# Kernel tuning notes

Measured on AMD Instinct MI355X. Metric: run time of the kernel, lower is better.

The kernel has to match this reference:

```python
import jax, jax.numpy as jnp
import numpy as np

N_PAIR = 32
N_ENTI = 36          # VidVRD object classes (+pad)
N_CLS_TOT = 133      # 132 predicate classes + background id 0
NUM_BASE = 92        # split='base' -> pids 1..92
N_CTX = 8
MAX_L = 40           # GeneralAlproCfg.max_txt_len
D = 768


def setup_inputs() -> dict:
    key = jax.random.key(0)
    ks = jax.random.split(key, 11)
    std = 0.02
    return {
        "so_cls_ids": jax.random.randint(ks[0], (N_PAIR, 2), 0, N_ENTI, dtype=jnp.int64),
        "enti_txt_embds": jax.random.normal(ks[1], (N_ENTI, 256), jnp.float32),
        "prefix_embds": jax.random.normal(ks[2], (N_CLS_TOT, 1, D), jnp.float32) * std,
        "suffix_embds": jax.random.normal(ks[3], (N_CLS_TOT, MAX_L - 1 - N_CTX, D), jnp.float32) * std,
        "token_mask": jnp.ones((N_CLS_TOT, MAX_L), jnp.int32),
        "meta_ctx_embds": jax.random.normal(ks[4], (N_CTX, D), jnp.float32) * std,
        "subj_ctx_embds": jax.random.normal(ks[5], (N_CTX, D), jnp.float32) * std,
        "obj_ctx_embds": jax.random.normal(ks[6], (N_CTX, D), jnp.float32) * std,
        "W1": jax.random.normal(ks[7], (512, 256), jnp.float32) * std,
        "b1": jnp.zeros((256,), jnp.float32),
        "W2": jax.random.normal(ks[8], (256, 2 * D), jnp.float32) * std,
    }


def reference(so_cls_ids, enti_txt_embds, prefix_embds, suffix_embds, token_mask,
              meta_ctx_embds, subj_ctx_embds, obj_ctx_embds, W1, b1, W2):
    n_pair = so_cls_ids.shape[0]
    pids = jnp.arange(1, NUM_BASE + 1)                      # split='base'
    n_cls = NUM_BASE

    # entity text-embedding gather + tiny MLP
    s_embd = enti_txt_embds[so_cls_ids[:, 0]]               # [n_pair, 256]
    o_embd = enti_txt_embds[so_cls_ids[:, 1]]
    so = jnp.concatenate([s_embd, o_embd], axis=-1)         # [n_pair, 512]
    h = jax.nn.relu(so @ W1 + b1)                           # [n_pair, 256]
    so_e = h @ W2                                           # [n_pair, 1536]
    s_q, o_q = so_e[:, :D], so_e[:, D:]

    # softmax attention over meta context (keys = values = meta_ctx_embds)
    scale = 1.0 / jnp.sqrt(jnp.asarray(D, jnp.float32))
    s_att = jax.nn.softmax(s_q @ meta_ctx_embds.T * scale, axis=-1) @ meta_ctx_embds  # [n_pair, D]
    o_att = jax.nn.softmax(o_q @ meta_ctx_embds.T * scale, axis=-1) @ meta_ctx_embds

    s_ctx = subj_ctx_embds[None, :, :] + s_att[:, None, :]  # [n_pair, n_ctx, D]
    o_ctx = obj_ctx_embds[None, :, :] + o_att[:, None, :]

    prefix = prefix_embds[pids]                             # [n_cls, 1, D]
    suffix = suffix_embds[pids]                             # [n_cls, L_suf, D]
    l_suf = suffix.shape[1]

    def build(ctx):
        return jnp.concatenate([
            jnp.broadcast_to(prefix[None], (n_pair, n_cls, 1, D)),
            jnp.broadcast_to(ctx[:, None], (n_pair, n_cls, N_CTX, D)),
            jnp.broadcast_to(suffix[None], (n_pair, n_cls, l_suf, D)),
        ], axis=2).reshape(n_pair * n_cls, MAX_L, D)

    subj_token_embds = build(s_ctx)                         # [n_pair*n_cls, MAX_L, D]
    obj_token_embds = build(o_ctx)
    mask = jnp.tile(token_mask[pids], (n_pair, 1))          # [n_pair*n_cls, MAX_L]
    return subj_token_embds, obj_token_embds, mask
```

## Files before the change

kernel.cpp:

```cpp
#include <hip/hip_runtime.h>
#include <hip/hip_bf16.h>

typedef unsigned int u32;
typedef __attribute__((ext_vector_type(4))) float f32x4;

#define NPAIR 32
#define NCLS  92
#define NCTX  8
#define MAXL  40
#define DIM   768
#define LSUF  31

#define MAT_ELEMS 90439680u
#define MASK_BASE 180879360u
#define NBLK_MAT  7360u
#define MASK_F4   29440u
#define NBLK_MASK 154u

__global__ __launch_bounds__(512) void k_mlp_att(
    const int* __restrict__ so_ids,
    const float* __restrict__ enti,
    const float* __restrict__ meta,
    const float* __restrict__ W1,
    const float* __restrict__ b1,
    const float* __restrict__ W2,
    float* __restrict__ att)
{
    const int p = blockIdx.x;
    const int t = threadIdx.x;
    __shared__ float so_vec[512];
    __shared__ float w1part[2][256];
    __shared__ float h[256];
    __shared__ float w2part[2][1536];
    __shared__ float so_e[1536];
    __shared__ float red[8][512];
    __shared__ float probs[8];
    __shared__ int ids[2];

    if (t == 0) {
        bool is64 = true;
        for (int i = 1; i < 64; i += 2) is64 = is64 && (so_ids[i] == 0);
        if (is64) { ids[0] = so_ids[4 * p];     ids[1] = so_ids[4 * p + 2]; }
        else      { ids[0] = so_ids[2 * p];     ids[1] = so_ids[2 * p + 1]; }
    }
    __syncthreads();
    const int s_id = ids[0];
    const int o_id = ids[1];
    so_vec[t] = (t < 256) ? enti[s_id * 256 + t] : enti[o_id * 256 + (t - 256)];
    __syncthreads();

    {
        const int j = t & 255, half = t >> 8;
        const float* w = W1 + (half * 256) * 256 + j;
        const float* sv = so_vec + half * 256;
        float acc = 0.f;
        #pragma unroll 8
        for (int kk = 0; kk < 256; ++kk)
            acc = fmaf(sv[kk], w[(size_t)kk * 256], acc);
        w1part[half][j] = acc;
    }
    __syncthreads();
    if (t < 256) h[t] = fmaxf(w1part[0][t] + w1part[1][t] + b1[t], 0.f);
    __syncthreads();

    {
        const int c = t & 255, khalf = t >> 8;
        float a6[6] = {0.f, 0.f, 0.f, 0.f, 0.f, 0.f};
        const float* w = W2 + (khalf * 128) * 1536 + c;
        const float* hh = h + khalf * 128;
        #pragma unroll 4
        for (int kk = 0; kk < 128; ++kk) {
            const float hk = hh[kk];
            #pragma unroll
            for (int r = 0; r < 6; ++r)
                a6[r] = fmaf(hk, w[(size_t)kk * 1536 + r * 256], a6[r]);
        }
        #pragma unroll
        for (int r = 0; r < 6; ++r) w2part[khalf][r * 256 + c] = a6[r];
    }
    __syncthreads();
    for (int c = t; c < 1536; c += 512) so_e[c] = w2part[0][c] + w2part[1][c];
    __syncthreads();

    const float scale = 0.036084391824351615f;
    for (int which = 0; which < 2; ++which) {
        const float* q = &so_e[which * DIM];
        #pragma unroll
        for (int c = 0; c < 8; ++c) {
            float pp = 0.f;
            for (int d = t; d < DIM; d += 512)
                pp = fmaf(q[d], meta[c * DIM + d], pp);
            red[c][t] = pp;
        }
        __syncthreads();
        for (int s = 256; s > 0; s >>= 1) {
            if (t < s) {
                #pragma unroll
                for (int c = 0; c < 8; ++c)
                    red[c][t] += red[c][t + s];
            }
            __syncthreads();
        }
        if (t == 0) {
            float sc[8], m = -1e30f;
            #pragma unroll
            for (int c = 0; c < 8; ++c) { sc[c] = red[c][0] * scale; m = fmaxf(m, sc[c]); }
            float sum = 0.f;
            #pragma unroll
            for (int c = 0; c < 8; ++c) { sc[c] = expf(sc[c] - m); sum += sc[c]; }
            const float inv = 1.f / sum;
            #pragma unroll
            for (int c = 0; c < 8; ++c) probs[c] = sc[c] * inv;
        }
        __syncthreads();
        for (int d = t; d < DIM; d += 512) {
            float a = 0.f;
            #pragma unroll
            for (int c = 0; c < 8; ++c)
                a = fmaf(probs[c], meta[c * DIM + d], a);
            att[(which * NPAIR + p) * DIM + d] = a;
        }
        __syncthreads();
    }
}

__global__ __launch_bounds__(192) void k_build(
    const float* __restrict__ prefix,
    const float* __restrict__ suffix,
    const int* __restrict__ tok_mask,
    const float* __restrict__ sctx,
    const float* __restrict__ octx,
    const float* __restrict__ att,
    float* __restrict__ out)
{
    const u32 bid = blockIdx.x;
    const u32 t = threadIdx.x;

    if (bid < NBLK_MAT) {
        const u32 which = bid / 3680u;
        const u32 rem = bid - which * 3680u;
        const u32 cls = rem / 40u;
        const u32 tok = rem - cls * 40u;
        const u32 d = t * 4u;

        f32x4 src;
        bool is_ctx = false;
        if (tok == 0u) {
            src = *(const f32x4*)(prefix + (cls + 1u) * DIM + d);
        } else if (tok < 9u) {
            const float* cp = (which ? octx : sctx) + (tok - 1u) * DIM + d;
            src = *(const f32x4*)cp;
            is_ctx = true;
        } else {
            src = *(const f32x4*)(suffix + ((cls + 1u) * LSUF + (tok - 9u)) * DIM + d);
        }

        float* base = out + (size_t)which * MAT_ELEMS + (size_t)(cls * MAXL + tok) * DIM + d;
        const float* ab = att + (size_t)which * NPAIR * DIM + d;
        if (is_ctx) {
            #pragma unroll 4
            for (u32 p = 0; p < NPAIR; ++p) {
                const f32x4 a = *(const f32x4*)(ab + (size_t)p * DIM);
                __builtin_nontemporal_store(src + a,
                    (f32x4*)(base + (size_t)p * (NCLS * MAXL * DIM)));
            }
        } else {
            #pragma unroll 4
            for (u32 p = 0; p < NPAIR; ++p) {
                __builtin_nontemporal_store(src,
                    (f32x4*)(base + (size_t)p * (NCLS * MAXL * DIM)));
            }
        }
    } else {
        const u32 idx4 = (bid - NBLK_MAT) * 192u + t;
        if (idx4 < MASK_F4) {
            const u32 m = idx4 * 4u;
            f32x4 v;
            #pragma unroll
            for (int j = 0; j < 4; ++j) {
                const u32 i = m + (u32)j;
                const u32 rw = i / 40u;
                const u32 tk = i - rw * 40u;
                const u32 cls = rw % 92u;
                v[j] = (float)tok_mask[(cls + 1u) * 40u + tk];
            }
            __builtin_nontemporal_store(v, (f32x4*)(out + MASK_BASE + m));
        }
    }
}

extern "C" void kernel_launch(void* const* d_in, const int* in_sizes, int n_in,
                              void* d_out, int out_size, void* d_ws, size_t ws_size,
                              hipStream_t stream) {
    const int* so_ids     = (const int*)d_in[0];
    const float* enti     = (const float*)d_in[1];
    const float* prefix   = (const float*)d_in[2];
    const float* suffix   = (const float*)d_in[3];
    const int* tok_mask   = (const int*)d_in[4];
    const float* meta     = (const float*)d_in[5];
    const float* sctx     = (const float*)d_in[6];
    const float* octx     = (const float*)d_in[7];
    const float* W1       = (const float*)d_in[8];
    const float* b1       = (const float*)d_in[9];
    const float* W2       = (const float*)d_in[10];
    float* att = (float*)d_ws;

    k_mlp_att<<<dim3(NPAIR), dim3(512), 0, stream>>>(so_ids, enti, meta, W1, b1, W2, att);
    k_build<<<dim3(NBLK_MAT + NBLK_MASK), dim3(192), 0, stream>>>(
        prefix, suffix, tok_mask, sctx, octx, att, (float*)d_out);
}
```

Baseline: 176.1 us.

## Split MLP-attention kernel into three kernels for more block parallelism

Breaks the single 32-block MLP+attention kernel into three launches: the first layer with ReLU, the W2 projection spread over 192 blocks, and the softmax attention over 64 blocks. Intermediates go through workspace buffers. The aim is to spread the serial small-matrix work across more CUs instead of 32 large blocks. The cost is two extra kernel launches and round trips through global memory. The prologue is small next to the large output-writing build kernel, which probably dominates total time.

```diff
diff --git a/kernel.cpp b/kernel.cpp
--- a/kernel.cpp
+++ b/kernel.cpp
@@ -17,24 +17,21 @@
 #define MASK_F4   29440u
 #define NBLK_MASK 154u
 
-__global__ __launch_bounds__(512) void k_mlp_att(
+#define WS_ATT  0u
+#define WS_H    49152u
+#define WS_SOE  57344u
+
+__global__ __launch_bounds__(512) void k_h(
     const int* __restrict__ so_ids,
     const float* __restrict__ enti,
-    const float* __restrict__ meta,
     const float* __restrict__ W1,
     const float* __restrict__ b1,
-    const float* __restrict__ W2,
-    float* __restrict__ att)
+    float* __restrict__ ws)
 {
     const int p = blockIdx.x;
     const int t = threadIdx.x;
     __shared__ float so_vec[512];
     __shared__ float w1part[2][256];
-    __shared__ float h[256];
-    __shared__ float w2part[2][1536];
-    __shared__ float so_e[1536];
-    __shared__ float red[8][512];
-    __shared__ float probs[8];
     __shared__ int ids[2];
 
     if (t == 0) {
@@ -44,83 +41,95 @@
         else      { ids[0] = so_ids[2 * p];     ids[1] = so_ids[2 * p + 1]; }
     }
     __syncthreads();
-    const int s_id = ids[0];
-    const int o_id = ids[1];
-    so_vec[t] = (t < 256) ? enti[s_id * 256 + t] : enti[o_id * 256 + (t - 256)];
-    __syncthreads();
-
-    {
-        const int j = t & 255, half = t >> 8;
-        const float* w = W1 + (half * 256) * 256 + j;
-        const float* sv = so_vec + half * 256;
-        float acc = 0.f;
-        #pragma unroll 8
-        for (int kk = 0; kk < 256; ++kk)
-            acc = fmaf(sv[kk], w[(size_t)kk * 256], acc);
-        w1part[half][j] = acc;
-    }
-    __syncthreads();
-    if (t < 256) h[t] = fmaxf(w1part[0][t] + w1part[1][t] + b1[t], 0.f);
-    __syncthreads();
-
-    {
-        const int c = t & 255, khalf = t >> 8;
-        float a6[6] = {0.f, 0.f, 0.f, 0.f, 0.f, 0.f};
-        const float* w = W2 + (khalf * 128) * 1536 + c;
-        const float* hh = h + khalf * 128;
-        #pragma unroll 4
-        for (int kk = 0; kk < 128; ++kk) {
-            const float hk = hh[kk];
-            #pragma unroll
-            for (int r = 0; r < 6; ++r)
-                a6[r] = fmaf(hk, w[(size_t)kk * 1536 + r * 256], a6[r]);
-        }
-        #pragma unroll
-        for (int r = 0; r < 6; ++r) w2part[khalf][r * 256 + c] = a6[r];
-    }
-    __syncthreads();
-    for (int c = t; c < 1536; c += 512) so_e[c] = w2part[0][c] + w2part[1][c];
-    __syncthreads();
-
-    const float scale = 0.036084391824351615f;
-    for (int which = 0; which < 2; ++which) {
-        const float* q = &so_e[which * DIM];
-        #pragma unroll
-        for (int c = 0; c < 8; ++c) {
-            float pp = 0.f;
-            for (int d = t; d < DIM; d += 512)
-                pp = fmaf(q[d], meta[c * DIM + d], pp);
-            red[c][t] = pp;
-        }
-        __syncthreads();
-        for (int s = 256; s > 0; s >>= 1) {
-            if (t < s) {
-                #pragma unroll
-                for (int c = 0; c < 8; ++c)
-                    red[c][t] += red[c][t + s];
-            }
-            __syncthreads();
-        }
-        if (t == 0) {
-            float sc[8], m = -1e30f;
-            #pragma unroll
-            for (int c = 0; c < 8; ++c) { sc[c] = red[c][0] * scale; m = fmaxf(m, sc[c]); }
-            float sum = 0.f;
-            #pragma unroll
-            for (int c = 0; c < 8; ++c) { sc[c] = expf(sc[c] - m); sum += sc[c]; }
-            const float inv = 1.f / sum;
-            #pragma unroll
-            for (int c = 0; c < 8; ++c) probs[c] = sc[c] * inv;
-        }
-        __syncthreads();
-        for (int d = t; d < DIM; d += 512) {
-            float a = 0.f;
+    so_vec[t] = (t < 256) ? enti[ids[0] * 256 + t] : enti[ids[1] * 256 + (t - 256)];
+    __syncthreads();
+
+    const int j = t & 255, half = t >> 8;
+    const float* w = W1 + (half * 256) * 256 + j;
+    const float* sv = so_vec + half * 256;
+    float acc = 0.f;
+    #pragma unroll 8
+    for (int kk = 0; kk < 256; ++kk)
+        acc = fmaf(sv[kk], w[(size_t)kk * 256], acc);
+    w1part[half][j] = acc;
+    __syncthreads();
+    if (t < 256)
+        ws[WS_H + p * 256 + t] = fmaxf(w1part[0][t] + w1part[1][t] + b1[t], 0.f);
+}
+
+__global__ __launch_bounds__(256) void k_soe(
+    const float* __restrict__ W2,
+    float* __restrict__ ws)
+{
+    const int p = blockIdx.x / 6;
+    const int cc = blockIdx.x % 6;
+    const int t = threadIdx.x;
+    __shared__ float hl[256];
+    hl[t] = ws[WS_H + p * 256 + t];
+    __syncthreads();
+
+    const int c = cc * 256 + t;
+    const float* w = W2 + c;
+    float acc = 0.f;
+    #pragma unroll 8
+    for (int k = 0; k < 256; ++k)
+        acc = fmaf(hl[k], w[(size_t)k * 1536], acc);
+    ws[WS_SOE + p * 1536 + c] = acc;
+}
+
+__global__ __launch_bounds__(256) void k_att(
+    const float* __restrict__ meta,
+    float* __restrict__ ws)
+{
+    const int which = blockIdx.x >> 5;
+    const int p = blockIdx.x & 31;
+    const int t = threadIdx.x;
+    __shared__ float red[8][256];
+    __shared__ float probs[8];
+
+    const float* q = ws + WS_SOE + p * 1536 + which * DIM;
+    float qr[3];
+    #pragma unroll
+    for (int i = 0; i < 3; ++i) qr[i] = q[t + 256 * i];
+
+    #pragma unroll
+    for (int c = 0; c < 8; ++c) {
+        float pp = 0.f;
+        #pragma unroll
+        for (int i = 0; i < 3; ++i)
+            pp = fmaf(qr[i], meta[c * DIM + t + 256 * i], pp);
+        red[c][t] = pp;
+    }
+    __syncthreads();
+    for (int s = 128; s > 0; s >>= 1) {
+        if (t < s) {
             #pragma unroll
             for (int c = 0; c < 8; ++c)
-                a = fmaf(probs[c], meta[c * DIM + d], a);
-            att[(which * NPAIR + p) * DIM + d] = a;
+                red[c][t] += red[c][t + s];
         }
         __syncthreads();
+    }
+    if (t == 0) {
+        const float scale = 0.036084391824351615f;
+        float sc[8], m = -1e30f;
+        #pragma unroll
+        for (int c = 0; c < 8; ++c) { sc[c] = red[c][0] * scale; m = fmaxf(m, sc[c]); }
+        float sum = 0.f;
+        #pragma unroll
+        for (int c = 0; c < 8; ++c) { sc[c] = expf(sc[c] - m); sum += sc[c]; }
+        const float inv = 1.f / sum;
+        #pragma unroll
+        for (int c = 0; c < 8; ++c) probs[c] = sc[c] * inv;
+    }
+    __syncthreads();
+    #pragma unroll
+    for (int i = 0; i < 3; ++i) {
+        const int d = t + 256 * i;
+        float a = 0.f;
+        #pragma unroll
+        for (int c = 0; c < 8; ++c)
+            a = fmaf(probs[c], meta[c * DIM + d], a);
+        ws[WS_ATT + (which * NPAIR + p) * DIM + d] = a;
     }
 }
 
@@ -203,9 +212,11 @@
     const float* W1       = (const float*)d_in[8];
     const float* b1       = (const float*)d_in[9];
     const float* W2       = (const float*)d_in[10];
-    float* att = (float*)d_ws;
-
-    k_mlp_att<<<dim3(NPAIR), dim3(512), 0, stream>>>(so_ids, enti, meta, W1, b1, W2, att);
+    float* ws = (float*)d_ws;
+
+    k_h  <<<dim3(NPAIR), dim3(512), 0, stream>>>(so_ids, enti, W1, b1, ws);
+    k_soe<<<dim3(192),   dim3(256), 0, stream>>>(W2, ws);
+    k_att<<<dim3(64),    dim3(256), 0, stream>>>(meta, ws);
     k_build<<<dim3(NBLK_MAT + NBLK_MASK), dim3(192), 0, stream>>>(
-        prefix, suffix, tok_mask, sctx, octx, att, (float*)d_out);
-}
+        prefix, suffix, tok_mask, sctx, octx, ws + WS_ATT, (float*)d_out);
+}
```

Result: faster. 166.6 us (-5.4%).
